# Kernel optimization log

Hardware: AMD Instinct MI355X
Metric: run time of the kernel (lower is better)

Reference implementation:

```python
import jax, jax.numpy as jnp
import numpy as np

N = 50000          # nodes
E = 1_000_000      # edges
NODE_DIM = 16
EMB = 64           # embed_dim
OUT = 64           # out_dim per head
EA_DIM = 8         # raw edge_attr_dim
HEADS = 8
SLOPE = 0.01       # leaky_relu default negative slope
LN_EPS = 1e-5


def mlp(x, w, b, g, beta):
    # MLP(in, out): Linear -> LayerNorm -> ReLU (standard block in this repo)
    y = x @ w + b
    mu = jnp.mean(y, axis=-1, keepdims=True)
    var = jnp.var(y, axis=-1, keepdims=True)
    y = (y - mu) / jnp.sqrt(var + LN_EPS) * g + beta
    return jax.nn.relu(y)


def gat_layer(x, ea, src, tgt, W, a):
    """AA_GATlayer forward (dropout = identity at eval).
    x: [N, in], ea: [E, EMB], W: [in, OUT], a: [2*OUT + EMB]."""
    h = x @ W                                  # [N, OUT]
    d = h.shape[1]
    a_src, a_tgt, a_edge = a[:d], a[d:2 * d], a[2 * d:]
    # score = leaky_relu(a @ concat([h_src, h_tgt, ea])) without materializing the concat
    s = jax.nn.leaky_relu(h[src] @ a_src + h[tgt] @ a_tgt + ea @ a_edge, SLOPE)  # [E]
    s = s - jnp.max(s)
    e = jnp.exp(s)
    denom = jax.ops.segment_sum(e, src, num_segments=N)          # [N]
    attn = e / (denom[src] + 1e-16)                              # [E]
    h_prime = jax.ops.segment_sum(h[tgt] * attn[:, None], src, num_segments=N)  # [N, OUT]
    return jax.nn.elu(h_prime)


def setup_inputs() -> dict:
    key = jax.random.key(0)
    ks = jax.random.split(key, 16)
    sc = lambda fan_in: 1.0 / np.sqrt(fan_in)
    inp = {}
    inp["X"] = jax.random.normal(ks[0], (N, NODE_DIM), jnp.float32)
    inp["edge_attr"] = jax.random.normal(ks[1], (E, EA_DIM), jnp.float32)
    inp["edge_index"] = jax.random.randint(ks[2], (2, E), 0, N, jnp.int64)
    inp["matched_car_infra_nodes"] = jax.random.randint(ks[3], (1000,), 0, N, jnp.int64)
    # node_embed MLP params
    inp["w_node"] = jax.random.uniform(ks[4], (NODE_DIM, EMB), jnp.float32, -sc(NODE_DIM), sc(NODE_DIM))
    inp["b_node"] = jnp.zeros((EMB,), jnp.float32)
    inp["g_node"] = jnp.ones((EMB,), jnp.float32)
    inp["beta_node"] = jnp.zeros((EMB,), jnp.float32)
    # edge_attr_embed MLP params
    inp["w_edge"] = jax.random.uniform(ks[5], (EA_DIM, EMB), jnp.float32, -sc(EA_DIM), sc(EA_DIM))
    inp["b_edge"] = jnp.zeros((EMB,), jnp.float32)
    inp["g_edge"] = jnp.ones((EMB,), jnp.float32)
    inp["beta_edge"] = jnp.zeros((EMB,), jnp.float32)
    # 8 GAT heads: W [EMB,OUT], a [2*OUT+EMB]
    inp["gat_W"] = jax.random.uniform(ks[6], (HEADS, EMB, OUT), jnp.float32, -sc(EMB), sc(EMB))
    inp["gat_a"] = jax.random.uniform(ks[7], (HEADS, 2 * OUT + EMB), jnp.float32, -sc(2 * OUT + EMB), sc(2 * OUT + EMB))
    # output GAT layer: W [OUT*HEADS, OUT], a [2*OUT+EMB]
    inp["out_W"] = jax.random.uniform(ks[8], (OUT * HEADS, OUT), jnp.float32, -sc(OUT * HEADS), sc(OUT * HEADS))
    inp["out_a"] = jax.random.uniform(ks[9], (2 * OUT + EMB,), jnp.float32, -sc(2 * OUT + EMB), sc(2 * OUT + EMB))
    return inp


def reference(X, edge_attr, w_node, b_node, g_node, beta_node,
              w_edge, b_edge, g_edge, beta_edge,
              gat_W, gat_a, out_W, out_a,
              edge_index, matched_car_infra_nodes):
    src, tgt = edge_index[0], edge_index[1]
    x = mlp(X, w_node, b_node, g_node, beta_node)                  # [N, EMB]
    ea = mlp(edge_attr, w_edge, b_edge, g_edge, beta_edge)         # [E, EMB]
    heads = [gat_layer(x, ea, src, tgt, gat_W[i], gat_a[i]) for i in range(HEADS)]
    xh = jax.nn.elu(jnp.concatenate(heads, axis=1))                # [N, OUT*HEADS]
    out = gat_layer(xh, ea, src, tgt, out_W, out_a)                # [N, OUT]
    return jax.nn.log_softmax(out, axis=1)
```

## Files before the change

kernel.cpp:

```cpp
#include <hip/hip_runtime.h>
#include <hip/hip_fp16.h>

#define NN 50000
#define EE 1000000
#define EPT 4

typedef _Float16 h8v __attribute__((ext_vector_type(8)));
typedef float    f4a __attribute__((ext_vector_type(4)));
typedef float    f4v __attribute__((ext_vector_type(4)));

__device__ __forceinline__ float wsum(float v){
#pragma unroll
  for(int m=1;m<64;m<<=1) v += __shfl_xor(v,m,64);
  return v;
}
__device__ __forceinline__ unsigned encf(float f){
  unsigned u = __float_as_uint(f);
  return (u & 0x80000000u) ? ~u : (u | 0x80000000u);
}
__device__ __forceinline__ float decf(unsigned u){
  u = (u & 0x80000000u) ? (u & 0x7fffffffu) : ~u;
  return __uint_as_float(u);
}

__global__ __launch_bounds__(256) void prep_k(int* counts, int* cursor, unsigned* mx,
                                              const float* __restrict__ gat_W, const float* __restrict__ gat_a,
                                              const float* __restrict__ out_W, const float* __restrict__ out_a,
                                              float* __restrict__ cdir, __half* __restrict__ WT,
                                              __half* __restrict__ OT){
  int i = blockIdx.x*256 + threadIdx.x;
  if(i < NN){ counts[i] = 0; cursor[i] = 0; }
  if(i < 64) mx[i] = 0u;
  if(blockIdx.x < 8){
    int h = blockIdx.x, tid = threadIdx.x;
    if(tid < 64){
      const float* W = gat_W + (size_t)h*4096;
      const float* a = gat_a + (size_t)h*192;
      float cs = 0.f, ct = 0.f;
#pragma unroll
      for(int j=0;j<64;j++){ float wv = W[tid*64+j]; cs += wv*a[j]; ct += wv*a[64+j]; }
      cdir[h*64 + tid]       = cs;
      cdir[512 + h*64 + tid] = ct;
    }
    for(int idx = tid; idx < 4096; idx += 256){
      int j = idx >> 6, k = idx & 63;
      WT[(size_t)h*4096 + k*64 + j] = __float2half(gat_W[(size_t)h*4096 + j*64 + k]);
      OT[(size_t)h*4096 + k*64 + j] = __float2half(out_W[(size_t)h*4096 + j*64 + k]);
    }
  }
}

__global__ __launch_bounds__(256) void node_hist_k(const float* __restrict__ X, const float* __restrict__ w,
                                                   const float* __restrict__ b, const float* __restrict__ g,
                                                   const float* __restrict__ beta, const float* __restrict__ cdir,
                                                   __half* __restrict__ x, float* __restrict__ ps8,
                                                   float* __restrict__ pt8,
                                                   const int* __restrict__ src, int* __restrict__ counts){
  const int NB_N = (NN*64 + 255)/256;
  if(blockIdx.x >= NB_N){
    int e = (blockIdx.x - NB_N)*256 + threadIdx.x;
    if(e < EE){
      int s = src[e];
      if((unsigned)s >= NN) s = 0;
      atomicAdd(&counts[s], 1);
    }
    return;
  }
  int wid  = (blockIdx.x*256 + threadIdx.x) >> 6;
  int lane = threadIdx.x & 63;
  if(wid >= NN) return;
  float acc = b[lane];
#pragma unroll
  for(int k=0;k<16;k++) acc += X[wid*16+k] * w[k*64+lane];
  float mu  = wsum(acc) * (1.0f/64.0f);
  float d   = acc - mu;
  float var = wsum(d*d) * (1.0f/64.0f);
  float y   = d * rsqrtf(var + 1e-5f) * g[lane] + beta[lane];
  float xv  = fmaxf(y, 0.0f);
  x[(size_t)wid*64 + lane] = __float2half(xv);
#pragma unroll 1
  for(int h=0;h<8;h++){
    float a = wsum(xv * cdir[h*64+lane]);
    float c = wsum(xv * cdir[512 + h*64+lane]);
    if(lane == 0){ ps8[wid*8+h] = a; pt8[wid*8+h] = c; }
  }
}

#define SCH 49
__global__ __launch_bounds__(1024) void scan_k(const int* __restrict__ counts, int* __restrict__ offs){
  __shared__ int sm[1024];
  int t = threadIdx.x;
  int base = t*SCH;
  int loc[SCH];
  int sum = 0;
#pragma unroll
  for(int i=0;i<SCH;i++){
    int idx = base+i;
    int v = (idx < NN) ? counts[idx] : 0;
    loc[i] = sum; sum += v;
  }
  sm[t] = sum; __syncthreads();
  for(int off=1; off<1024; off<<=1){
    int u = (t >= off) ? sm[t-off] : 0;
    __syncthreads();
    sm[t] += u;
    __syncthreads();
  }
  int ex = (t == 0) ? 0 : sm[t-1];
#pragma unroll
  for(int i=0;i<SCH;i++){
    int idx = base+i;
    if(idx < NN) offs[idx] = ex + loc[i];
  }
  if(t == 0) offs[NN] = EE;
}

__global__ __launch_bounds__(256) void scatter_k(const int* __restrict__ src, const int* __restrict__ tgt,
                                                 const int* __restrict__ offs, int* __restrict__ cursor,
                                                 int* __restrict__ rank, int* __restrict__ tgt_s,
                                                 int* __restrict__ src_s){
  int e = blockIdx.x*blockDim.x + threadIdx.x;
  if(e < EE){
    int s = src[e];
    if((unsigned)s >= NN) s = 0;
    int pos = offs[s] + atomicAdd(&cursor[s], 1);
    rank[e] = pos;
    int t = tgt[e];
    if((unsigned)t >= NN) t = 0;
    tgt_s[pos] = t;
    src_s[pos] = s;
  }
}

__global__ __launch_bounds__(256, 2) void edge_mlp_q(const int* __restrict__ rank, const float* __restrict__ ea,
                                                  const float* __restrict__ w, const float* __restrict__ b,
                                                  const float* __restrict__ g, const float* __restrict__ beta,
                                                  const float* __restrict__ gat_a, const float* __restrict__ out_a,
                                                  __half* __restrict__ q8h, float* __restrict__ q_out,
                                                  unsigned* __restrict__ mx){
  __shared__ float P[64*20];
  __shared__ float smx[4][9];
  int tid = threadIdx.x;
  for(int idx=tid; idx<1280; idx+=256){
    int j = idx/20, c = idx - j*20;
    float v;
    if(c < 8)       v = w[c*64+j];
    else if(c == 8) v = b[j];
    else if(c == 9) v = g[j];
    else if(c ==10) v = beta[j];
    else if(c ==11) v = out_a[128+j];
    else            v = gat_a[(c-12)*192 + 128 + j];
    P[idx] = v;
  }
  __syncthreads();
  int base = blockIdx.x*(256*EPT) + tid;
  float4 ia[EPT], ib[EPT];
  bool  vl[EPT];
#pragma unroll
  for(int k=0;k<EPT;k++){
    int e = base + k*256;
    vl[k] = (e < EE);
    size_t es = vl[k] ? (size_t)e : 0;
    ia[k] = ((const float4*)ea)[es*2];
    ib[k] = ((const float4*)ea)[es*2+1];
  }
  float s1[EPT], s2[EPT];
#pragma unroll
  for(int k=0;k<EPT;k++){ s1[k]=0.f; s2[k]=0.f; }
#pragma unroll 4
  for(int j=0;j<64;j++){
    float4 w0 = *(const float4*)&P[j*20];
    float4 w1 = *(const float4*)&P[j*20+4];
    float4 c4 = *(const float4*)&P[j*20+8];
#pragma unroll
    for(int k=0;k<EPT;k++){
      float acc = c4.x;
      acc = fmaf(ia[k].x,w0.x, fmaf(ia[k].y,w0.y, fmaf(ia[k].z,w0.z, fmaf(ia[k].w,w0.w, acc))));
      acc = fmaf(ib[k].x,w1.x, fmaf(ib[k].y,w1.y, fmaf(ib[k].z,w1.z, fmaf(ib[k].w,w1.w, acc))));
      s1[k] += acc;
      s2[k] = fmaf(acc,acc,s2[k]);
    }
  }
  float mu[EPT], inv[EPT];
#pragma unroll
  for(int k=0;k<EPT;k++){
    mu[k]  = s1[k]*(1.0f/64.0f);
    float var = fmaxf(s2[k]*(1.0f/64.0f) - mu[k]*mu[k], 0.0f);
    inv[k] = rsqrtf(var + 1e-5f);
  }
  float qv[EPT][9];
#pragma unroll
  for(int k=0;k<EPT;k++)
#pragma unroll
    for(int r=0;r<9;r++) qv[k][r]=0.f;
#pragma unroll 4
  for(int j=0;j<64;j++){
    float4 w0 = *(const float4*)&P[j*20];
    float4 w1 = *(const float4*)&P[j*20+4];
    float4 c4 = *(const float4*)&P[j*20+8];
    float4 a0 = *(const float4*)&P[j*20+12];
    float4 a1 = *(const float4*)&P[j*20+16];
#pragma unroll
    for(int k=0;k<EPT;k++){
      float acc = c4.x;
      acc = fmaf(ia[k].x,w0.x, fmaf(ia[k].y,w0.y, fmaf(ia[k].z,w0.z, fmaf(ia[k].w,w0.w, acc))));
      acc = fmaf(ib[k].x,w1.x, fmaf(ib[k].y,w1.y, fmaf(ib[k].z,w1.z, fmaf(ib[k].w,w1.w, acc))));
      float yj = fmaxf(fmaf((acc - mu[k])*inv[k], c4.y, c4.z), 0.0f);
      qv[k][0]=fmaf(yj,a0.x,qv[k][0]); qv[k][1]=fmaf(yj,a0.y,qv[k][1]);
      qv[k][2]=fmaf(yj,a0.z,qv[k][2]); qv[k][3]=fmaf(yj,a0.w,qv[k][3]);
      qv[k][4]=fmaf(yj,a1.x,qv[k][4]); qv[k][5]=fmaf(yj,a1.y,qv[k][5]);
      qv[k][6]=fmaf(yj,a1.z,qv[k][6]); qv[k][7]=fmaf(yj,a1.w,qv[k][7]);
      qv[k][8]=fmaf(yj,c4.w,qv[k][8]);
    }
  }
  float mq[9];
#pragma unroll
  for(int r=0;r<9;r++) mq[r] = -3.0e38f;
#pragma unroll
  for(int k=0;k<EPT;k++){
    if(vl[k]){
      int e = base + k*256;
      int rk = rank[e];
      __half2 p01 = __floats2half2_rn(qv[k][0],qv[k][1]);
      __half2 p23 = __floats2half2_rn(qv[k][2],qv[k][3]);
      __half2 p45 = __floats2half2_rn(qv[k][4],qv[k][5]);
      __half2 p67 = __floats2half2_rn(qv[k][6],qv[k][7]);
      uint4 pk;
      pk.x = *(unsigned*)&p01; pk.y = *(unsigned*)&p23;
      pk.z = *(unsigned*)&p45; pk.w = *(unsigned*)&p67;
      *(uint4*)(q8h + (size_t)rk*8) = pk;
      q_out[rk] = qv[k][8];
#pragma unroll
      for(int r=0;r<9;r++) mq[r] = fmaxf(mq[r], qv[k][r]);
    }
  }
#pragma unroll
  for(int r=0;r<9;r++)
#pragma unroll
    for(int m=1;m<64;m<<=1) mq[r] = fmaxf(mq[r], __shfl_xor(mq[r],m,64));
  int wv = tid>>6, lane = tid&63;
  if(lane == 0){
#pragma unroll
    for(int r=0;r<9;r++) smx[wv][r] = mq[r];
  }
  __syncthreads();
  if(tid < 9){
    float v = fmaxf(fmaxf(smx[0][tid],smx[1][tid]), fmaxf(smx[2][tid],smx[3][tid]));
    atomicMax(&mx[tid], encf(v));
  }
}

__global__ __launch_bounds__(256) void maxp_k(const float* __restrict__ ps8, const float* __restrict__ pt8,
                                              unsigned* __restrict__ mx){
  float m[16];
#pragma unroll
  for(int r=0;r<16;r++) m[r] = -3.0e38f;
  for(int i = blockIdx.x*256 + threadIdx.x; i < NN; i += gridDim.x*256){
    float4 a = ((const float4*)ps8)[(size_t)i*2];
    float4 c = ((const float4*)ps8)[(size_t)i*2+1];
    float4 d = ((const float4*)pt8)[(size_t)i*2];
    float4 e = ((const float4*)pt8)[(size_t)i*2+1];
    m[0]=fmaxf(m[0],a.x); m[1]=fmaxf(m[1],a.y); m[2]=fmaxf(m[2],a.z); m[3]=fmaxf(m[3],a.w);
    m[4]=fmaxf(m[4],c.x); m[5]=fmaxf(m[5],c.y); m[6]=fmaxf(m[6],c.z); m[7]=fmaxf(m[7],c.w);
    m[8]=fmaxf(m[8],d.x); m[9]=fmaxf(m[9],d.y); m[10]=fmaxf(m[10],d.z); m[11]=fmaxf(m[11],d.w);
    m[12]=fmaxf(m[12],e.x); m[13]=fmaxf(m[13],e.y); m[14]=fmaxf(m[14],e.z); m[15]=fmaxf(m[15],e.w);
  }
#pragma unroll
  for(int r=0;r<16;r++)
#pragma unroll
    for(int msk=1;msk<64;msk<<=1) m[r] = fmaxf(m[r], __shfl_xor(m[r],msk,64));
  __shared__ float sm[4][16];
  int wv = threadIdx.x>>6, lane = threadIdx.x&63;
  if(lane == 0){
#pragma unroll
    for(int r=0;r<16;r++) sm[wv][r] = m[r];
  }
  __syncthreads();
  if(threadIdx.x < 16){
    int r = threadIdx.x;
    float v = fmaxf(fmaxf(sm[0][r],sm[1][r]), fmaxf(sm[2][r],sm[3][r]));
    atomicMax(&mx[16+r], encf(v));
  }
}

__global__ __launch_bounds__(256) void maxpo_k(const float* __restrict__ ps_o, const float* __restrict__ pt_o,
                                               unsigned* __restrict__ mx){
  float m0 = -3.0e38f, m1 = -3.0e38f;
  for(int i = blockIdx.x*256 + threadIdx.x; i < NN; i += gridDim.x*256){
    m0 = fmaxf(m0, ps_o[i]); m1 = fmaxf(m1, pt_o[i]);
  }
#pragma unroll
  for(int msk=1;msk<64;msk<<=1){ m0=fmaxf(m0,__shfl_xor(m0,msk,64)); m1=fmaxf(m1,__shfl_xor(m1,msk,64)); }
  __shared__ float sm[4][2];
  int wv = threadIdx.x>>6, lane = threadIdx.x&63;
  if(lane == 0){ sm[wv][0]=m0; sm[wv][1]=m1; }
  __syncthreads();
  if(threadIdx.x < 2){
    int r = threadIdx.x;
    float v = fmaxf(fmaxf(sm[0][r],sm[1][r]), fmaxf(sm[2][r],sm[3][r]));
    atomicMax(&mx[32+r], encf(v));
  }
}

__global__ __launch_bounds__(256) void score_k(const int* __restrict__ src_s, const int* __restrict__ tgt_s,
                                               const float* __restrict__ ps8, const float* __restrict__ pt8,
                                               const unsigned* __restrict__ mx, const __half* __restrict__ q8h,
                                               __half* __restrict__ w8h){
  int i = blockIdx.x*256 + threadIdx.x;
  if(i >= EE) return;
  int s = src_s[i], t = tgt_s[i];
  uint4 rq = *(const uint4*)(q8h + (size_t)i*8);
  float2 q01 = __half22float2(*(const __half2*)&rq.x);
  float2 q23 = __half22float2(*(const __half2*)&rq.y);
  float2 q45 = __half22float2(*(const __half2*)&rq.z);
  float2 q67 = __half22float2(*(const __half2*)&rq.w);
  float4 sa = ((const float4*)ps8)[(size_t)s*2];
  float4 sb = ((const float4*)ps8)[(size_t)s*2+1];
  float4 ta = ((const float4*)pt8)[(size_t)t*2];
  float4 tb = ((const float4*)pt8)[(size_t)t*2+1];
  float sv[8] = {q01.x+sa.x+ta.x, q01.y+sa.y+ta.y, q23.x+sa.z+ta.z, q23.y+sa.w+ta.w,
                 q45.x+sb.x+tb.x, q45.y+sb.y+tb.y, q67.x+sb.z+tb.z, q67.y+sb.w+tb.w};
  float wv[8];
#pragma unroll
  for(int h=0;h<8;h++){
    float B = decf(mx[h]) + decf(mx[16+h]) + decf(mx[24+h]);
    float M = (B > 0.f) ? B : 0.01f*B;
    float x = sv[h];
    x = (x > 0.f) ? x : 0.01f*x;
    wv[h] = __expf(x - M);
  }
  __half2 p01 = __floats2half2_rn(wv[0],wv[1]);
  __half2 p23 = __floats2half2_rn(wv[2],wv[3]);
  __half2 p45 = __floats2half2_rn(wv[4],wv[5]);
  __half2 p67 = __floats2half2_rn(wv[6],wv[7]);
  uint4 pk;
  pk.x = *(unsigned*)&p01; pk.y = *(unsigned*)&p23;
  pk.z = *(unsigned*)&p45; pk.w = *(unsigned*)&p67;
  *(uint4*)(w8h + (size_t)i*8) = pk;
}

__global__ __launch_bounds__(256) void agg_k(const int* __restrict__ offs, const int* __restrict__ tgt_s,
    const __half* __restrict__ w8h, const __half* __restrict__ x, __half* __restrict__ pre){
  int wid  = (blockIdx.x*blockDim.x + threadIdx.x) >> 6;
  int lane = threadIdx.x & 63;
  int quad = lane >> 4, l16 = lane & 15;
  int b  = offs[wid];
  int e2 = offs[wid+1];
  float  den[8];
  float4 num[8];
#pragma unroll
  for(int h=0;h<8;h++){ den[h] = 0.f; num[h] = make_float4(0.f,0.f,0.f,0.f); }
  for(int i=b+quad; i<e2; i+=4){
    int t = tgt_s[i];
    uint4 rw = *(const uint4*)(w8h + (size_t)i*8);
    float2 w01 = __half22float2(*(const __half2*)&rw.x);
    float2 w23 = __half22float2(*(const __half2*)&rw.y);
    float2 w45 = __half22float2(*(const __half2*)&rw.z);
    float2 w67 = __half22float2(*(const __half2*)&rw.w);
    uint2 raw = *(const uint2*)(x + (size_t)t*64 + l16*4);
    float2 fa = __half22float2(*(const __half2*)&raw.x);
    float2 fb = __half22float2(*(const __half2*)&raw.y);
    float4 xv = make_float4(fa.x, fa.y, fb.x, fb.y);
    float wv[8] = {w01.x,w01.y,w23.x,w23.y, w45.x,w45.y,w67.x,w67.y};
#pragma unroll
    for(int h=0;h<8;h++){
      den[h]   += wv[h];
      num[h].x = fmaf(wv[h],xv.x,num[h].x); num[h].y = fmaf(wv[h],xv.y,num[h].y);
      num[h].z = fmaf(wv[h],xv.z,num[h].z); num[h].w = fmaf(wv[h],xv.w,num[h].w);
    }
  }
#pragma unroll
  for(int h=0;h<8;h++){
    den[h]   += __shfl_xor(den[h],16,64);   den[h]   += __shfl_xor(den[h],32,64);
    num[h].x += __shfl_xor(num[h].x,16,64); num[h].x += __shfl_xor(num[h].x,32,64);
    num[h].y += __shfl_xor(num[h].y,16,64); num[h].y += __shfl_xor(num[h].y,32,64);
    num[h].z += __shfl_xor(num[h].z,16,64); num[h].z += __shfl_xor(num[h].z,32,64);
    num[h].w += __shfl_xor(num[h].w,16,64); num[h].w += __shfl_xor(num[h].w,32,64);
  }
  __half* dst = pre + (size_t)wid*512;
#pragma unroll
  for(int k=0;k<2;k++){
    int h = 2*quad + k;
    float invd = (den[h] > 0.f) ? 1.0f/den[h] : 0.f;
    __half2 h0 = __floats2half2_rn(num[h].x*invd, num[h].y*invd);
    __half2 h1 = __floats2half2_rn(num[h].z*invd, num[h].w*invd);
    uint2 pk; pk.x = *(unsigned*)&h0; pk.y = *(unsigned*)&h1;
    *(uint2*)(dst + h*64 + l16*4) = pk;
  }
}

__global__ __launch_bounds__(256) void transform_mfma(const __half* __restrict__ pre,
                                                      const __half* __restrict__ WT,
                                                      const __half* __restrict__ OT,
                                                      float* __restrict__ h2p){
  __shared__ __half zl[4*16*64];
  int tid = threadIdx.x;
  int w  = tid >> 6, l = tid & 63;
  int lr = l & 15, lg = l >> 4;
  int n0 = blockIdx.x * 64;
  int g  = blockIdx.y;
  h2p += (size_t)g * NN * 64;
  int gn  = n0 + w*16 + lr;
  int gnr = (gn < NN) ? gn : 0;
  __half* zw = zl + w*1024;
  f4a out[4];
#pragma unroll
  for(int i=0;i<4;i++){ out[i][0]=0.f; out[i][1]=0.f; out[i][2]=0.f; out[i][3]=0.f; }
#pragma unroll 1
  for(int hh=0; hh<4; hh++){
    int h = g*4 + hh;
    h8v a1_0 = *(const h8v*)(pre + (size_t)gnr*512 + h*64 + 0*32 + lg*8);
    h8v a1_1 = *(const h8v*)(pre + (size_t)gnr*512 + h*64 + 1*32 + lg*8);
    f4a zacc[4];
#pragma unroll
    for(int nt=0; nt<4; nt++){ zacc[nt][0]=0.f; zacc[nt][1]=0.f; zacc[nt][2]=0.f; zacc[nt][3]=0.f; }
    const __half* WTh = WT + (size_t)h*4096;
#pragma unroll
    for(int nt=0; nt<4; nt++){
      h8v b0 = *(const h8v*)(WTh + (nt*16 + lr)*64 + 0*32 + lg*8);
      h8v b1 = *(const h8v*)(WTh + (nt*16 + lr)*64 + 1*32 + lg*8);
      zacc[nt] = __builtin_amdgcn_mfma_f32_16x16x32_f16(a1_0, b0, zacc[nt], 0, 0, 0);
      zacc[nt] = __builtin_amdgcn_mfma_f32_16x16x32_f16(a1_1, b1, zacc[nt], 0, 0, 0);
    }
#pragma unroll
    for(int nt=0; nt<4; nt++){
#pragma unroll
      for(int r=0; r<4; r++){
        float v = zacc[nt][r];
        float z = (v > 0.f) ? v : expm1f(v);
        z = (z > 0.f) ? z : expm1f(z);
        int rho = lg*4 + r;
        int c   = nt*16 + lr;
        int pc  = (((c>>3) ^ (rho&7))<<3) | (c&7);
        zw[rho*64 + pc] = __float2half(z);
      }
    }
    const __half* OTh = OT + (size_t)h*4096;
#pragma unroll
    for(int ks=0; ks<2; ks++){
      int Gp = (lg + 4*ks) ^ (lr & 7);
      h8v a2 = *(const h8v*)(zw + lr*64 + Gp*8);
#pragma unroll
      for(int nt=0; nt<4; nt++){
        h8v b2 = *(const h8v*)(OTh + (nt*16 + lr)*64 + ks*32 + lg*8);
        out[nt] = __builtin_amdgcn_mfma_f32_16x16x32_f16(a2, b2, out[nt], 0, 0, 0);
      }
    }
  }
#pragma unroll
  for(int nt=0; nt<4; nt++){
#pragma unroll
    for(int r=0; r<4; r++){
      int grow = n0 + w*16 + lg*4 + r;
      if(grow < NN) h2p[(size_t)grow*64 + nt*16 + lr] = out[nt][r];
    }
  }
}

__global__ __launch_bounds__(256) void finalize_po(const float* __restrict__ p0, const float* __restrict__ p1,
                                                   const float* __restrict__ out_a, __half* __restrict__ h2f,
                                                   float* __restrict__ ps_o, float* __restrict__ pt_o){
  int wid  = (blockIdx.x*blockDim.x + threadIdx.x) >> 6;
  int lane = threadIdx.x & 63;
  if(wid >= NN) return;
  float v = p0[(size_t)wid*64 + lane] + p1[(size_t)wid*64 + lane];
  float ps = wsum(v * out_a[lane]);
  float pt = wsum(v * out_a[64+lane]);
  if(lane == 0){ ps_o[wid] = ps; pt_o[wid] = pt; }
  h2f[(size_t)wid*64 + lane] = __float2half(v);
}

__global__ __launch_bounds__(256) void agg_out(const int* __restrict__ offs, const int* __restrict__ tgt_s,
                                               const float* __restrict__ q_out, const float* __restrict__ ps_o,
                                               const float* __restrict__ pt_o, const unsigned* __restrict__ mx,
                                               const __half* __restrict__ h2f, float* __restrict__ dout){
  int wid  = (blockIdx.x*blockDim.x + threadIdx.x) >> 6;
  int lane = threadIdx.x & 63;
  if(wid >= NN) return;
  int quad = lane >> 4, l16 = lane & 15;
  int b  = offs[wid];
  int e2 = offs[wid+1];
  float B = decf(mx[8]) + decf(mx[32]) + decf(mx[33]);
  float M = (B > 0.f) ? B : 0.01f*B;
  float pso = ps_o[wid];
  float4 num = make_float4(0.f,0.f,0.f,0.f);
  float den = 0.f;
  for(int i=b+quad; i<e2; i+=4){
    int t = tgt_s[i];
    float sv = q_out[i] + pso + pt_o[t];
    sv = (sv > 0.f) ? sv : 0.01f*sv;
    float w = __expf(sv - M);
    uint2 raw = *(const uint2*)(h2f + (size_t)t*64 + l16*4);
    float2 fa = __half22float2(*(const __half2*)&raw.x);
    float2 fb = __half22float2(*(const __half2*)&raw.y);
    den += w;
    num.x = fmaf(w,fa.x,num.x); num.y = fmaf(w,fa.y,num.y);
    num.z = fmaf(w,fb.x,num.z); num.w = fmaf(w,fb.y,num.w);
  }
  den   += __shfl_xor(den,16,64);   den   += __shfl_xor(den,32,64);
  num.x += __shfl_xor(num.x,16,64); num.x += __shfl_xor(num.x,32,64);
  num.y += __shfl_xor(num.y,16,64); num.y += __shfl_xor(num.y,32,64);
  num.z += __shfl_xor(num.z,16,64); num.z += __shfl_xor(num.z,32,64);
  num.w += __shfl_xor(num.w,16,64); num.w += __shfl_xor(num.w,32,64);
  float inv = (den > 0.f) ? 1.0f/den : 0.f;
  float z[4];
  float mloc = -3.0e38f;
#pragma unroll
  for(int k=0;k<4;k++){
    float hp = ((&num.x)[k]) * inv;
    z[k] = (hp > 0.f) ? hp : expm1f(hp);
    mloc = fmaxf(mloc, z[k]);
  }
#pragma unroll
  for(int msk=1; msk<16; msk<<=1) mloc = fmaxf(mloc, __shfl_xor(mloc,msk,64));
  float ssum = 0.f;
#pragma unroll
  for(int k=0;k<4;k++) ssum += __expf(z[k] - mloc);
#pragma unroll
  for(int msk=1; msk<16; msk<<=1) ssum += __shfl_xor(ssum,msk,64);
  float lse = mloc + logf(ssum);
  if(quad == 0){
    f4v o; o.x = z[0]-lse; o.y = z[1]-lse; o.z = z[2]-lse; o.w = z[3]-lse;
    __builtin_nontemporal_store(o, (f4v*)(dout + (size_t)wid*64 + l16*4));
  }
}

extern "C" void kernel_launch(void* const* d_in, const int* in_sizes, int n_in,
                              void* d_out, int out_size, void* d_ws, size_t ws_size,
                              hipStream_t stream) {
  const float* X         = (const float*)d_in[0];
  const float* edge_attr = (const float*)d_in[1];
  const int*   edge_index= (const int*)d_in[2];
  const float* w_node    = (const float*)d_in[4];
  const float* b_node    = (const float*)d_in[5];
  const float* g_node    = (const float*)d_in[6];
  const float* beta_node = (const float*)d_in[7];
  const float* w_edge    = (const float*)d_in[8];
  const float* b_edge    = (const float*)d_in[9];
  const float* g_edge    = (const float*)d_in[10];
  const float* beta_edge = (const float*)d_in[11];
  const float* gat_W     = (const float*)d_in[12];
  const float* gat_a     = (const float*)d_in[13];
  const float* out_W     = (const float*)d_in[14];
  const float* out_a     = (const float*)d_in[15];
  float* dout = (float*)d_out;

  const int* src = edge_index;
  const int* tgt = edge_index + EE;

  char* base = (char*)d_ws;
  size_t off = 0;
  auto take = [&](size_t bytes)->char*{ char* p = base + off; off += (bytes + 31) & ~(size_t)31; return p; };
  int*      counts = (int*)     take((size_t)NN*4);
  int*      cursor = (int*)     take((size_t)NN*4);
  int*      offs   = (int*)     take((size_t)(NN+1)*4);
  unsigned* mx     = (unsigned*)take(64*4);
  float*    ps_o   = (float*)   take((size_t)NN*4);
  float*    pt_o   = (float*)   take((size_t)NN*4);
  float*    cdir   = (float*)   take(1024*4);
  int*      rank   = (int*)     take((size_t)EE*4);
  int*      tgt_s  = (int*)     take((size_t)EE*4);
  int*      src_s  = (int*)     take((size_t)EE*4);
  float*    ps8    = (float*)   take((size_t)NN*8*4);
  float*    pt8    = (float*)   take((size_t)NN*8*4);
  __half*   xh     = (__half*)  take((size_t)NN*64*2);
  __half*   h2fh   = (__half*)  take((size_t)NN*64*2);
  __half*   WT16   = (__half*)  take((size_t)8*4096*2);
  __half*   OT16   = (__half*)  take((size_t)8*4096*2);
  float*    h2p    = (float*)   take((size_t)2*NN*64*4);
  __half*   q8h    = (__half*)  take((size_t)EE*8*2);
  __half*   w8h    = (__half*)  take((size_t)EE*8*2);
  float*    q_out  = (float*)   take((size_t)EE*4);
  __half*   pre    = (__half*)  take((size_t)NN*512*2);

  const int NBLK_N  = (NN*64 + 255)/256;
  const int NBLK_E  = (EE + 255)/256;
  const int NBLK_EM = (EE + 256*EPT - 1)/(256*EPT);
  const int NBLK_S  = (NN + 255)/256;
  const int NBLK_A  = (NN + 3)/4;
  const int NBLK_T  = (NN + 63)/64;

  prep_k     <<<NBLK_S, 256, 0, stream>>>(counts, cursor, mx, gat_W, gat_a, out_W, out_a,
                                          cdir, WT16, OT16);
  node_hist_k<<<NBLK_N + NBLK_E, 256, 0, stream>>>(X, w_node, b_node, g_node, beta_node, cdir,
                                                   xh, ps8, pt8, src, counts);
  scan_k     <<<1,     1024, 0, stream>>>(counts, offs);
  scatter_k  <<<NBLK_E, 256, 0, stream>>>(src, tgt, offs, cursor, rank, tgt_s, src_s);
  edge_mlp_q <<<NBLK_EM,256, 0, stream>>>(rank, edge_attr, w_edge, b_edge, g_edge, beta_edge,
                                          gat_a, out_a, q8h, q_out, mx);
  maxp_k     <<<128,    256, 0, stream>>>(ps8, pt8, mx);
  score_k    <<<NBLK_E, 256, 0, stream>>>(src_s, tgt_s, ps8, pt8, mx, q8h, w8h);
  agg_k      <<<NBLK_A, 256, 0, stream>>>(offs, tgt_s, w8h, xh, pre);
  {
    dim3 tg((unsigned)NBLK_T, 2);
    transform_mfma<<<tg, 256, 0, stream>>>(pre, WT16, OT16, h2p);
  }
  finalize_po<<<NBLK_N, 256, 0, stream>>>(h2p, h2p + (size_t)NN*64, out_a, h2fh, ps_o, pt_o);
  maxpo_k    <<<128,  256, 0, stream>>>(ps_o, pt_o, mx);
  agg_out    <<<NBLK_N,256, 0, stream>>>(offs, tgt_s, q_out, ps_o, pt_o, mx, h2fh, dout);
}
```

Baseline: 680.9 us.

## Split aggregation kernels into two passes by target-node half for cache locality

Both the hidden-layer and output-layer aggregation kernels are split into two launches. Each launch only gathers from target nodes in one half of the node range, so the gathered feature rows should fit better in L2/MALL. The first pass writes unnormalized partial numerators and denominators; the second adds its partials to them and applies normalization, ELU and log-softmax. This trades an extra read of the CSR edge list and tgt_s, plus partial-result traffic, for better gather locality. It also stores pre in fp16 before normalization, which may lose precision, and drops the nontemporal output store.

```diff
diff --git a/kernel.cpp b/kernel.cpp
--- a/kernel.cpp
+++ b/kernel.cpp
@@ -3,6 +3,7 @@
 
 #define NN 50000
 #define EE 1000000
+#define NHALF 25000
 #define EPT 4
 
 typedef _Float16 h8v __attribute__((ext_vector_type(8)));
@@ -339,8 +340,9 @@
   *(uint4*)(w8h + (size_t)i*8) = pk;
 }
 
-__global__ __launch_bounds__(256) void agg_k(const int* __restrict__ offs, const int* __restrict__ tgt_s,
-    const __half* __restrict__ w8h, const __half* __restrict__ x, __half* __restrict__ pre){
+__global__ __launch_bounds__(256) void agg_p0(const int* __restrict__ offs, const int* __restrict__ tgt_s,
+    const __half* __restrict__ w8h, const __half* __restrict__ x, __half* __restrict__ pre,
+    float* __restrict__ denp){
   int wid  = (blockIdx.x*blockDim.x + threadIdx.x) >> 6;
   int lane = threadIdx.x & 63;
   int quad = lane >> 4, l16 = lane & 15;
@@ -352,21 +354,23 @@
   for(int h=0;h<8;h++){ den[h] = 0.f; num[h] = make_float4(0.f,0.f,0.f,0.f); }
   for(int i=b+quad; i<e2; i+=4){
     int t = tgt_s[i];
-    uint4 rw = *(const uint4*)(w8h + (size_t)i*8);
-    float2 w01 = __half22float2(*(const __half2*)&rw.x);
-    float2 w23 = __half22float2(*(const __half2*)&rw.y);
-    float2 w45 = __half22float2(*(const __half2*)&rw.z);
-    float2 w67 = __half22float2(*(const __half2*)&rw.w);
-    uint2 raw = *(const uint2*)(x + (size_t)t*64 + l16*4);
-    float2 fa = __half22float2(*(const __half2*)&raw.x);
-    float2 fb = __half22float2(*(const __half2*)&raw.y);
-    float4 xv = make_float4(fa.x, fa.y, fb.x, fb.y);
-    float wv[8] = {w01.x,w01.y,w23.x,w23.y, w45.x,w45.y,w67.x,w67.y};
-#pragma unroll
-    for(int h=0;h<8;h++){
-      den[h]   += wv[h];
-      num[h].x = fmaf(wv[h],xv.x,num[h].x); num[h].y = fmaf(wv[h],xv.y,num[h].y);
-      num[h].z = fmaf(wv[h],xv.z,num[h].z); num[h].w = fmaf(wv[h],xv.w,num[h].w);
+    if(t < NHALF){
+      uint4 rw = *(const uint4*)(w8h + (size_t)i*8);
+      float2 w01 = __half22float2(*(const __half2*)&rw.x);
+      float2 w23 = __half22float2(*(const __half2*)&rw.y);
+      float2 w45 = __half22float2(*(const __half2*)&rw.z);
+      float2 w67 = __half22float2(*(const __half2*)&rw.w);
+      uint2 raw = *(const uint2*)(x + (size_t)t*64 + l16*4);
+      float2 fa = __half22float2(*(const __half2*)&raw.x);
+      float2 fb = __half22float2(*(const __half2*)&raw.y);
+      float4 xv = make_float4(fa.x, fa.y, fb.x, fb.y);
+      float wv[8] = {w01.x,w01.y,w23.x,w23.y, w45.x,w45.y,w67.x,w67.y};
+#pragma unroll
+      for(int h=0;h<8;h++){
+        den[h]   += wv[h];
+        num[h].x = fmaf(wv[h],xv.x,num[h].x); num[h].y = fmaf(wv[h],xv.y,num[h].y);
+        num[h].z = fmaf(wv[h],xv.z,num[h].z); num[h].w = fmaf(wv[h],xv.w,num[h].w);
+      }
     }
   }
 #pragma unroll
@@ -381,9 +385,68 @@
 #pragma unroll
   for(int k=0;k<2;k++){
     int h = 2*quad + k;
-    float invd = (den[h] > 0.f) ? 1.0f/den[h] : 0.f;
-    __half2 h0 = __floats2half2_rn(num[h].x*invd, num[h].y*invd);
-    __half2 h1 = __floats2half2_rn(num[h].z*invd, num[h].w*invd);
+    __half2 h0 = __floats2half2_rn(num[h].x, num[h].y);
+    __half2 h1 = __floats2half2_rn(num[h].z, num[h].w);
+    uint2 pk; pk.x = *(unsigned*)&h0; pk.y = *(unsigned*)&h1;
+    *(uint2*)(dst + h*64 + l16*4) = pk;
+    if(l16 == 0) denp[wid*8 + h] = den[h];
+  }
+}
+
+__global__ __launch_bounds__(256) void agg_p1(const int* __restrict__ offs, const int* __restrict__ tgt_s,
+    const __half* __restrict__ w8h, const __half* __restrict__ x, __half* __restrict__ pre,
+    const float* __restrict__ denp){
+  int wid  = (blockIdx.x*blockDim.x + threadIdx.x) >> 6;
+  int lane = threadIdx.x & 63;
+  int quad = lane >> 4, l16 = lane & 15;
+  int b  = offs[wid];
+  int e2 = offs[wid+1];
+  float  den[8];
+  float4 num[8];
+#pragma unroll
+  for(int h=0;h<8;h++){ den[h] = 0.f; num[h] = make_float4(0.f,0.f,0.f,0.f); }
+  for(int i=b+quad; i<e2; i+=4){
+    int t = tgt_s[i];
+    if(t >= NHALF){
+      uint4 rw = *(const uint4*)(w8h + (size_t)i*8);
+      float2 w01 = __half22float2(*(const __half2*)&rw.x);
+      float2 w23 = __half22float2(*(const __half2*)&rw.y);
+      float2 w45 = __half22float2(*(const __half2*)&rw.z);
+      float2 w67 = __half22float2(*(const __half2*)&rw.w);
+      uint2 raw = *(const uint2*)(x + (size_t)t*64 + l16*4);
+      float2 fa = __half22float2(*(const __half2*)&raw.x);
+      float2 fb = __half22float2(*(const __half2*)&raw.y);
+      float4 xv = make_float4(fa.x, fa.y, fb.x, fb.y);
+      float wv[8] = {w01.x,w01.y,w23.x,w23.y, w45.x,w45.y,w67.x,w67.y};
+#pragma unroll
+      for(int h=0;h<8;h++){
+        den[h]   += wv[h];
+        num[h].x = fmaf(wv[h],xv.x,num[h].x); num[h].y = fmaf(wv[h],xv.y,num[h].y);
+        num[h].z = fmaf(wv[h],xv.z,num[h].z); num[h].w = fmaf(wv[h],xv.w,num[h].w);
+      }
+    }
+  }
+#pragma unroll
+  for(int h=0;h<8;h++){
+    den[h]   += __shfl_xor(den[h],16,64);   den[h]   += __shfl_xor(den[h],32,64);
+    num[h].x += __shfl_xor(num[h].x,16,64); num[h].x += __shfl_xor(num[h].x,32,64);
+    num[h].y += __shfl_xor(num[h].y,16,64); num[h].y += __shfl_xor(num[h].y,32,64);
+    num[h].z += __shfl_xor(num[h].z,16,64); num[h].z += __shfl_xor(num[h].z,32,64);
+    num[h].w += __shfl_xor(num[h].w,16,64); num[h].w += __shfl_xor(num[h].w,32,64);
+  }
+  __half* dst = pre + (size_t)wid*512;
+#pragma unroll
+  for(int k=0;k<2;k++){
+    int h = 2*quad + k;
+    uint2 rp = *(const uint2*)(dst + h*64 + l16*4);
+    float2 pa = __half22float2(*(const __half2*)&rp.x);
+    float2 pb = __half22float2(*(const __half2*)&rp.y);
+    float dtot = den[h] + denp[wid*8 + h];
+    float nx = num[h].x + pa.x, ny = num[h].y + pa.y;
+    float nz = num[h].z + pb.x, nw = num[h].w + pb.y;
+    float invd = (dtot > 0.f) ? 1.0f/dtot : 0.f;
+    __half2 h0 = __floats2half2_rn(nx*invd, ny*invd);
+    __half2 h1 = __floats2half2_rn(nz*invd, nw*invd);
     uint2 pk; pk.x = *(unsigned*)&h0; pk.y = *(unsigned*)&h1;
     *(uint2*)(dst + h*64 + l16*4) = pk;
   }
@@ -470,10 +533,11 @@
   h2f[(size_t)wid*64 + lane] = __float2half(v);
 }
 
-__global__ __launch_bounds__(256) void agg_out(const int* __restrict__ offs, const int* __restrict__ tgt_s,
+__global__ __launch_bounds__(256) void aggo_p0(const int* __restrict__ offs, const int* __restrict__ tgt_s,
                                                const float* __restrict__ q_out, const float* __restrict__ ps_o,
                                                const float* __restrict__ pt_o, const unsigned* __restrict__ mx,
-                                               const __half* __restrict__ h2f, float* __restrict__ dout){
+                                               const __half* __restrict__ h2f, float* __restrict__ doutp,
+                                               float* __restrict__ deno){
   int wid  = (blockIdx.x*blockDim.x + threadIdx.x) >> 6;
   int lane = threadIdx.x & 63;
   if(wid >= NN) return;
@@ -487,21 +551,69 @@
   float den = 0.f;
   for(int i=b+quad; i<e2; i+=4){
     int t = tgt_s[i];
-    float sv = q_out[i] + pso + pt_o[t];
-    sv = (sv > 0.f) ? sv : 0.01f*sv;
-    float w = __expf(sv - M);
-    uint2 raw = *(const uint2*)(h2f + (size_t)t*64 + l16*4);
-    float2 fa = __half22float2(*(const __half2*)&raw.x);
-    float2 fb = __half22float2(*(const __half2*)&raw.y);
-    den += w;
-    num.x = fmaf(w,fa.x,num.x); num.y = fmaf(w,fa.y,num.y);
-    num.z = fmaf(w,fb.x,num.z); num.w = fmaf(w,fb.y,num.w);
+    if(t < NHALF){
+      float sv = q_out[i] + pso + pt_o[t];
+      sv = (sv > 0.f) ? sv : 0.01f*sv;
+      float w = __expf(sv - M);
+      uint2 raw = *(const uint2*)(h2f + (size_t)t*64 + l16*4);
+      float2 fa = __half22float2(*(const __half2*)&raw.x);
+      float2 fb = __half22float2(*(const __half2*)&raw.y);
+      den += w;
+      num.x = fmaf(w,fa.x,num.x); num.y = fmaf(w,fa.y,num.y);
+      num.z = fmaf(w,fb.x,num.z); num.w = fmaf(w,fb.y,num.w);
+    }
   }
   den   += __shfl_xor(den,16,64);   den   += __shfl_xor(den,32,64);
   num.x += __shfl_xor(num.x,16,64); num.x += __shfl_xor(num.x,32,64);
   num.y += __shfl_xor(num.y,16,64); num.y += __shfl_xor(num.y,32,64);
   num.z += __shfl_xor(num.z,16,64); num.z += __shfl_xor(num.z,32,64);
   num.w += __shfl_xor(num.w,16,64); num.w += __shfl_xor(num.w,32,64);
+  if(quad == 0){
+    ((float4*)doutp)[(size_t)wid*16 + l16] = num;
+    if(l16 == 0) deno[wid] = den;
+  }
+}
+
+__global__ __launch_bounds__(256) void aggo_p1(const int* __restrict__ offs, const int* __restrict__ tgt_s,
+                                               const float* __restrict__ q_out, const float* __restrict__ ps_o,
+                                               const float* __restrict__ pt_o, const unsigned* __restrict__ mx,
+                                               const __half* __restrict__ h2f, const float* __restrict__ deno,
+                                               float* __restrict__ dout){
+  int wid  = (blockIdx.x*blockDim.x + threadIdx.x) >> 6;
+  int lane = threadIdx.x & 63;
+  if(wid >= NN) return;
+  int quad = lane >> 4, l16 = lane & 15;
+  int b  = offs[wid];
+  int e2 = offs[wid+1];
+  float B = decf(mx[8]) + decf(mx[32]) + decf(mx[33]);
+  float M = (B > 0.f) ? B : 0.01f*B;
+  float pso = ps_o[wid];
+  float4 num = make_float4(0.f,0.f,0.f,0.f);
+  float den = 0.f;
+  for(int i=b+quad; i<e2; i+=4){
+    int t = tgt_s[i];
+    if(t >= NHALF){
+      float sv = q_out[i] + pso + pt_o[t];
+      sv = (sv > 0.f) ? sv : 0.01f*sv;
+      float w = __expf(sv - M);
+      uint2 raw = *(const uint2*)(h2f + (size_t)t*64 + l16*4);
+      float2 fa = __half22float2(*(const __half2*)&raw.x);
+      float2 fb = __half22float2(*(const __half2*)&raw.y);
+      den += w;
+      num.x = fmaf(w,fa.x,num.x); num.y = fmaf(w,fa.y,num.y);
+      num.z = fmaf(w,fb.x,num.z); num.w = fmaf(w,fb.y,num.w);
+    }
+  }
+  den   += __shfl_xor(den,16,64);   den   += __shfl_xor(den,32,64);
+  num.x += __shfl_xor(num.x,16,64); num.x += __shfl_xor(num.x,32,64);
+  num.y += __shfl_xor(num.y,16,64); num.y += __shfl_xor(num.y,32,64);
+  num.z += __shfl_xor(num.z,16,64); num.z += __shfl_xor(num.z,32,64);
+  num.w += __shfl_xor(num.w,16,64); num.w += __shfl_xor(num.w,32,64);
+  if(quad == 0){
+    float4 p = ((const float4*)dout)[(size_t)wid*16 + l16];
+    num.x += p.x; num.y += p.y; num.z += p.z; num.w += p.w;
+    den   += deno[wid];
+  }
   float inv = (den > 0.f) ? 1.0f/den : 0.f;
   float z[4];
   float mloc = -3.0e38f;
@@ -520,8 +632,8 @@
   for(int msk=1; msk<16; msk<<=1) ssum += __shfl_xor(ssum,msk,64);
   float lse = mloc + logf(ssum);
   if(quad == 0){
-    f4v o; o.x = z[0]-lse; o.y = z[1]-lse; o.z = z[2]-lse; o.w = z[3]-lse;
-    __builtin_nontemporal_store(o, (f4v*)(dout + (size_t)wid*64 + l16*4));
+    float4 o = make_float4(z[0]-lse, z[1]-lse, z[2]-lse, z[3]-lse);
+    ((float4*)dout)[(size_t)wid*16 + l16] = o;
   }
 }
 
@@ -572,6 +684,8 @@
   __half*   w8h    = (__half*)  take((size_t)EE*8*2);
   float*    q_out  = (float*)   take((size_t)EE*4);
   __half*   pre    = (__half*)  take((size_t)NN*512*2);
+  float*    denp   = (float*)   take((size_t)NN*8*4);
+  float*    deno   = (float*)   take((size_t)NN*4);
 
   const int NBLK_N  = (NN*64 + 255)/256;
   const int NBLK_E  = (EE + 255)/256;
@@ -590,12 +704,14 @@
                                           gat_a, out_a, q8h, q_out, mx);
   maxp_k     <<<128,    256, 0, stream>>>(ps8, pt8, mx);
   score_k    <<<NBLK_E, 256, 0, stream>>>(src_s, tgt_s, ps8, pt8, mx, q8h, w8h);
-  agg_k      <<<NBLK_A, 256, 0, stream>>>(offs, tgt_s, w8h, xh, pre);
+  agg_p0     <<<NBLK_A, 256, 0, stream>>>(offs, tgt_s, w8h, xh, pre, denp);
+  agg_p1     <<<NBLK_A, 256, 0, stream>>>(offs, tgt_s, w8h, xh, pre, denp);
   {
     dim3 tg((unsigned)NBLK_T, 2);
     transform_mfma<<<tg, 256, 0, stream>>>(pre, WT16, OT16, h2p);
   }
   finalize_po<<<NBLK_N, 256, 0, stream>>>(h2p, h2p + (size_t)NN*64, out_a, h2fh, ps_o, pt_o);
   maxpo_k    <<<128,  256, 0, stream>>>(ps_o, pt_o, mx);
-  agg_out    <<<NBLK_N,256, 0, stream>>>(offs, tgt_s, q_out, ps_o, pt_o, mx, h2fh, dout);
-}
+  aggo_p0    <<<NBLK_N, 256, 0, stream>>>(offs, tgt_s, q_out, ps_o, pt_o, mx, h2fh, dout, deno);
+  aggo_p1    <<<NBLK_N, 256, 0, stream>>>(offs, tgt_s, q_out, ps_o, pt_o, mx, h2fh, deno, dout);
+}
```

New measurement: 841.6 us. 23.6% more time.
